# Kernel tuning notes

Measured on AMD Instinct MI355X. Metric: run time of the kernel, lower is better.

## Reference

```python
import jax, jax.numpy as jnp
import numpy as np

B, LQ, LK = 4, 256, 512
DQ, DK, DV = 512, 512, 512
H = 256
NEG = -1e6


def setup_inputs() -> dict:
    key = jax.random.key(0)
    ks = jax.random.split(key, 7)
    queries = jax.random.normal(ks[0], (B, LQ, DQ), dtype=jnp.float32)
    keys = jax.random.normal(ks[1], (B, LK, DK), dtype=jnp.float32)
    values = jax.random.normal(ks[2], (B, LK, DV), dtype=jnp.float32)
    valid_lens = jax.random.randint(ks[3], (B,), 1, LK + 1).astype(jnp.int32)
    # learned params (Linear without bias): store as (in, out) so x @ W matches torch x @ W.T
    Wq = jax.random.normal(ks[4], (DQ, H), dtype=jnp.float32) * (1.0 / np.sqrt(DQ))
    Wk = jax.random.normal(ks[5], (DK, H), dtype=jnp.float32) * (1.0 / np.sqrt(DK))
    wv = jax.random.normal(ks[6], (H,), dtype=jnp.float32) * (1.0 / np.sqrt(H))
    return {"queries": queries, "keys": keys, "values": values,
            "valid_lens": valid_lens, "Wq": Wq, "Wk": Wk, "wv": wv}


def reference(queries, keys, values, valid_lens, Wq, Wk, wv):
    q = jnp.einsum('bqd,dh->bqh', queries, Wq)          # (B,Lq,H)
    k = jnp.einsum('bkd,dh->bkh', keys, Wk)             # (B,Lk,H)
    feats = jnp.tanh(q[:, :, None, :] + k[:, None, :, :])  # (B,Lq,Lk,H)
    scores = jnp.einsum('bqkh,h->bqk', feats, wv)        # (B,Lq,Lk)
    mask = jnp.arange(LK)[None, None, :] < valid_lens[:, None, None]  # (B,1,Lk)
    attn = jax.nn.softmax(jnp.where(mask, scores, NEG), axis=-1)
    return jnp.einsum('bqk,bkv->bqv', attn, values)      # (B,Lq,Dv)
```

## Files before the change

### kernel.cpp

```cpp
#include <hip/hip_runtime.h>

#define B_   4
#define LQ_  256
#define LK_  512
#define DIN_ 512
#define H_   256
#define DV_  512

#define L2E 1.4426950408889634f

__global__ __launch_bounds__(256) void proj_partial_kernel(
    const float* __restrict__ Q, const float* __restrict__ K,
    const float* __restrict__ Wq, const float* __restrict__ Wk,
    const int* __restrict__ valid_lens,
    float* __restrict__ qpart, float* __restrict__ ekTpart) {
  __shared__ float xs[64][68];
  __shared__ float ws[64][132];

  const int blk = blockIdx.x;
  const bool isQ = blk < 128;
  int b, row0, h0, ds;
  if (isQ) {
    const int qi = blk;
    ds = qi & 3; h0 = ((qi >> 2) & 1) * 128;
    const int rt = qi >> 3;
    b = rt >> 2; row0 = (rt & 3) * 64;
  } else {
    const int u = blk - 128;
    ds = u & 3; h0 = ((u >> 2) & 1) * 128;
    const int rt = u >> 3;
    b = rt & 3; row0 = (rt >> 2) * 64;
    if (row0 >= valid_lens[b]) return;
  }
  const int L = isQ ? LQ_ : LK_;
  const float* __restrict__ X = (isQ ? Q : K) + ((size_t)(b * L + row0)) * DIN_ + ds * 128;
  const float* __restrict__ Wb = (isQ ? Wq : Wk) + (size_t)(ds * 128) * H_ + h0;

  const int t = threadIdx.x;
  const int hthr = t & 31;
  const int rthr = t >> 5;

  float acc[8][4];
#pragma unroll
  for (int r = 0; r < 8; ++r)
#pragma unroll
    for (int c = 0; c < 4; ++c) acc[r][c] = 0.f;

  for (int dd = 0; dd < 128; dd += 64) {
    __syncthreads();
#pragma unroll
    for (int u = 0; u < 4; ++u) {
      const int f = t + 256 * u;
      const int r = f >> 4, c4 = (f & 15) << 2;
      *(float4*)&xs[r][c4] = *(const float4*)&X[(size_t)r * DIN_ + dd + c4];
    }
#pragma unroll
    for (int u = 0; u < 8; ++u) {
      const int f = t + 256 * u;
      const int k = f >> 5, c4 = (f & 31) << 2;
      *(float4*)&ws[k][c4] = *(const float4*)&Wb[(size_t)(dd + k) * H_ + c4];
    }
    __syncthreads();

    for (int k = 0; k < 64; k += 8) {
      float4 w4[8];
#pragma unroll
      for (int k8 = 0; k8 < 8; ++k8)
        w4[k8] = *(const float4*)&ws[k + k8][4 * hthr];
#pragma unroll
      for (int rr = 0; rr < 8; ++rr) {
        const float4 xa = *(const float4*)&xs[rthr * 8 + rr][k];
        const float4 xb = *(const float4*)&xs[rthr * 8 + rr][k + 4];
        const float xv[8] = {xa.x, xa.y, xa.z, xa.w, xb.x, xb.y, xb.z, xb.w};
#pragma unroll
        for (int k8 = 0; k8 < 8; ++k8) {
          acc[rr][0] = fmaf(xv[k8], w4[k8].x, acc[rr][0]);
          acc[rr][1] = fmaf(xv[k8], w4[k8].y, acc[rr][1]);
          acc[rr][2] = fmaf(xv[k8], w4[k8].z, acc[rr][2]);
          acc[rr][3] = fmaf(xv[k8], w4[k8].w, acc[rr][3]);
        }
      }
    }
  }

  if (isQ) {
    float* dst = qpart + (size_t)ds * (B_ * LQ_ * H_);
#pragma unroll
    for (int rr = 0; rr < 8; ++rr) {
      const int row = row0 + rthr * 8 + rr;
      float4 o = {acc[rr][0], acc[rr][1], acc[rr][2], acc[rr][3]};
      *(float4*)&dst[(size_t)(b * LQ_ + row) * H_ + h0 + 4 * hthr] = o;
    }
  } else {
    float* dst = ekTpart + (size_t)ds * (B_ * H_ * LK_);
#pragma unroll
    for (int c = 0; c < 4; ++c) {
      const int h = h0 + 4 * hthr + c;
      float* p = &dst[((size_t)b * H_ + h) * LK_ + row0 + rthr * 8];
      float4 lo = {acc[0][c], acc[1][c], acc[2][c], acc[3][c]};
      float4 hi = {acc[4][c], acc[5][c], acc[6][c], acc[7][c]};
      *(float4*)p = lo;
      *(float4*)(p + 4) = hi;
    }
  }
}

__global__ __launch_bounds__(512) void combine_exp_kernel(
    const float* __restrict__ qpart, const float* __restrict__ ekTpart,
    const float* __restrict__ wv,
    float* __restrict__ eq, float* __restrict__ ekT, float* __restrict__ wsum) {
  const int idx = blockIdx.x * 512 + threadIdx.x;
  const int NQ4 = B_ * LQ_ * H_ / 4;
  const float4* src;
  float4* dst;
  size_t stride4;
  int k4;
  if (idx < NQ4) {
    src = (const float4*)qpart; dst = (float4*)eq;
    stride4 = NQ4; k4 = idx;
  } else {
    src = (const float4*)ekTpart; dst = (float4*)ekT;
    stride4 = B_ * H_ * LK_ / 4; k4 = idx - NQ4;
  }
  float4 a = src[k4];
  float4 b1 = src[stride4 + k4];
  float4 c = src[2 * stride4 + k4];
  float4 d = src[3 * stride4 + k4];
  float4 o;
  o.x = exp2f(fminf(fmaxf((a.x + b1.x + c.x + d.x) * L2E, -126.f), 126.f));
  o.y = exp2f(fminf(fmaxf((a.y + b1.y + c.y + d.y) * L2E, -126.f), 126.f));
  o.z = exp2f(fminf(fmaxf((a.z + b1.z + c.z + d.z) * L2E, -126.f), 126.f));
  o.w = exp2f(fminf(fmaxf((a.w + b1.w + c.w + d.w) * L2E, -126.f), 126.f));
  dst[k4] = o;

  if (blockIdx.x == 0 && threadIdx.x < 64) {
    const int t = threadIdx.x;
    float s = wv[t] + wv[t + 64] + wv[t + 128] + wv[t + 192];
#pragma unroll
    for (int off = 32; off; off >>= 1) s += __shfl_xor(s, off);
    if (t == 0) *wsum = s;
  }
}

__global__ __launch_bounds__(256) void scores_kernel(
    const float* __restrict__ eq, const float* __restrict__ ekT,
    const float* __restrict__ wv, const float* __restrict__ wsum,
    const int* __restrict__ valid_lens, float* __restrict__ sc) {
  const int blk = blockIdx.x;
  const int b  = blk & 3;
  const int i0 = ((blk >> 2) & 63) * 4;
  const int jc = blk >> 8;
  const int vl = valid_lens[b];
  if (jc * 256 >= vl) return;
  const int t = threadIdx.x;
  if (jc * 256 + ((t >> 6) << 6) >= vl) return;
  const int j = jc * 256 + t;

  const float* __restrict__ kcol = ekT + (size_t)b * H_ * LK_ + j;
  const float* __restrict__ q0 = eq + (size_t)(b * LQ_ + i0) * H_;
  const float Wsum = *wsum;

  float a0 = 0.f, a1 = 0.f, a2 = 0.f, a3 = 0.f;
  for (int h = 0; h < H_; h += 8) {
    float kv[8];
#pragma unroll
    for (int u = 0; u < 8; ++u) kv[u] = kcol[(size_t)(h + u) * LK_];
    const float4 wa = *(const float4*)&wv[h];
    const float4 wb = *(const float4*)&wv[h + 4];
    const float ww[8] = {wa.x, wa.y, wa.z, wa.w, wb.x, wb.y, wb.z, wb.w};
#pragma unroll
    for (int ii = 0; ii < 4; ++ii) {
      const float4 qa = *(const float4*)&q0[ii * H_ + h];
      const float4 qb = *(const float4*)&q0[ii * H_ + h + 4];
      const float qv[8] = {qa.x, qa.y, qa.z, qa.w, qb.x, qb.y, qb.z, qb.w};
      float* acc = (ii == 0) ? &a0 : (ii == 1) ? &a1 : (ii == 2) ? &a2 : &a3;
      float s = *acc;
#pragma unroll
      for (int u = 0; u < 8; ++u) {
        const float p = qv[u] * kv[u];
        s = fmaf(ww[u], __builtin_amdgcn_rcpf(fmaf(p, p, 1.f)), s);
      }
      *acc = s;
    }
  }
  const size_t o = (size_t)(b * LQ_ + i0) * LK_ + j;
  if (j < vl) {
    sc[o]           = fmaf(-2.f, a0, Wsum);
    sc[o + LK_]     = fmaf(-2.f, a1, Wsum);
    sc[o + 2 * LK_] = fmaf(-2.f, a2, Wsum);
    sc[o + 3 * LK_] = fmaf(-2.f, a3, Wsum);
  }
}

__global__ __launch_bounds__(512) void softmax_av_kernel(
    const float* __restrict__ sc, const float* __restrict__ V,
    const int* __restrict__ valid_lens, float* __restrict__ out) {
  __shared__ float4 p4s[LK_];
  __shared__ float redm[8][4];
  __shared__ float reds[8][4];

  const int blk = blockIdx.x;
  const int b = blk >> 6;
  const int i0 = (blk & 63) * 4;
  const int vl = valid_lens[b];
  const int t = threadIdx.x;
  const int lane = t & 63, wave = t >> 6;

  const float* __restrict__ srow = sc + (size_t)(b * LQ_ + i0) * LK_;
  const bool valid = t < vl;
  float s[4], m[4];
#pragma unroll
  for (int ii = 0; ii < 4; ++ii) {
    s[ii] = valid ? srow[ii * LK_ + t] : -3.0e38f;
    m[ii] = s[ii];
  }
#pragma unroll
  for (int off = 32; off; off >>= 1)
#pragma unroll
    for (int ii = 0; ii < 4; ++ii) m[ii] = fmaxf(m[ii], __shfl_xor(m[ii], off));
  if (lane == 0)
#pragma unroll
    for (int ii = 0; ii < 4; ++ii) redm[wave][ii] = m[ii];
  __syncthreads();
  float e[4], sum[4];
#pragma unroll
  for (int ii = 0; ii < 4; ++ii) {
    float mx = redm[0][ii];
#pragma unroll
    for (int w = 1; w < 8; ++w) mx = fmaxf(mx, redm[w][ii]);
    e[ii] = valid ? __expf(s[ii] - mx) : 0.f;
    sum[ii] = e[ii];
  }
#pragma unroll
  for (int off = 32; off; off >>= 1)
#pragma unroll
    for (int ii = 0; ii < 4; ++ii) sum[ii] += __shfl_xor(sum[ii], off);
  if (lane == 0)
#pragma unroll
    for (int ii = 0; ii < 4; ++ii) reds[wave][ii] = sum[ii];
  __syncthreads();
  {
    float4 pv;
    float tot[4];
#pragma unroll
    for (int ii = 0; ii < 4; ++ii) {
      tot[ii] = reds[0][ii];
#pragma unroll
      for (int w = 1; w < 8; ++w) tot[ii] += reds[w][ii];
    }
    pv.x = e[0] * __builtin_amdgcn_rcpf(tot[0]);
    pv.y = e[1] * __builtin_amdgcn_rcpf(tot[1]);
    pv.z = e[2] * __builtin_amdgcn_rcpf(tot[2]);
    pv.w = e[3] * __builtin_amdgcn_rcpf(tot[3]);
    p4s[t] = pv;
  }
  __syncthreads();

  const float* __restrict__ Vb = V + (size_t)b * LK_ * DV_ + t;
  float a[4] = {0.f, 0.f, 0.f, 0.f};
  int j = 0;
  const int jv = vl & ~7;
  for (; j < jv; j += 8) {
    float v[8];
#pragma unroll
    for (int u = 0; u < 8; ++u) v[u] = Vb[(size_t)(j + u) * DV_];
#pragma unroll
    for (int u = 0; u < 8; ++u) {
      const float4 pp = p4s[j + u];
      a[0] = fmaf(pp.x, v[u], a[0]); a[1] = fmaf(pp.y, v[u], a[1]);
      a[2] = fmaf(pp.z, v[u], a[2]); a[3] = fmaf(pp.w, v[u], a[3]);
    }
  }
  for (; j < vl; ++j) {
    const float v = Vb[(size_t)j * DV_];
    const float4 pp = p4s[j];
    a[0] = fmaf(pp.x, v, a[0]); a[1] = fmaf(pp.y, v, a[1]);
    a[2] = fmaf(pp.z, v, a[2]); a[3] = fmaf(pp.w, v, a[3]);
  }
#pragma unroll
  for (int ii = 0; ii < 4; ++ii)
    out[(size_t)(b * LQ_ + i0 + ii) * DV_ + t] = a[ii];
}

extern "C" void kernel_launch(void* const* d_in, const int* in_sizes, int n_in,
                              void* d_out, int out_size, void* d_ws, size_t ws_size,
                              hipStream_t stream) {
  const float* queries    = (const float*)d_in[0];
  const float* keys       = (const float*)d_in[1];
  const float* values     = (const float*)d_in[2];
  const int*   valid_lens = (const int*)d_in[3];
  const float* Wq         = (const float*)d_in[4];
  const float* Wk         = (const float*)d_in[5];
  const float* wv         = (const float*)d_in[6];
  float* out = (float*)d_out;

  char* ws = (char*)d_ws;
  float* qpart   = (float*)ws;
  float* ekTpart = (float*)(ws + (size_t)( 4 << 20));
  float* eq      = (float*)(ws + (size_t)(12 << 20));
  float* ekT     = (float*)(ws + (size_t)(13 << 20));
  float* sc      = (float*)(ws + (size_t)(15 << 20));
  float* wsum    = (float*)(ws + (size_t)(17 << 20));

  proj_partial_kernel<<<384, 256, 0, stream>>>(
      queries, keys, Wq, Wk, valid_lens, qpart, ekTpart);
  combine_exp_kernel<<<384, 512, 0, stream>>>(
      qpart, ekTpart, wv, eq, ekT, wsum);
  scores_kernel<<<512, 256, 0, stream>>>(
      eq, ekT, wv, wsum, valid_lens, sc);
  softmax_av_kernel<<<B_ * (LQ_ / 4), 512, 0, stream>>>(
      sc, values, valid_lens, out);
}
```

Before: 63.82 us.

## Tile scores kernel in LDS with 2x2 register blocking and row-major ek

The scores kernel now stages a 32x256 block of exp(q) and a transposed 32x256 block of exp(k) in shared memory, and each thread computes a 2x2 tile of scores. Previously each thread read a column of ekT from global memory and q rows through the cache. The projection kernel now writes exp(k) row-major like q, so the transposed global store is gone and the transpose happens in LDS instead. The code references a variable `L` that is not defined in the shown lines, and the scores kernel no longer masks j >= valid_len within a tile, which relies on softmax ignoring those entries.

```diff
diff --git a/kernel.cpp b/kernel.cpp
--- a/kernel.cpp
+++ b/kernel.cpp
@@ -13,7 +13,7 @@
     const float* __restrict__ Q, const float* __restrict__ K,
     const float* __restrict__ Wq, const float* __restrict__ Wk,
     const int* __restrict__ valid_lens,
-    float* __restrict__ qpart, float* __restrict__ ekTpart) {
+    float* __restrict__ qpart, float* __restrict__ ekpart) {
   __shared__ float xs[64][68];
   __shared__ float ws[64][132];
 
@@ -83,32 +83,20 @@
     }
   }
 
-  if (isQ) {
-    float* dst = qpart + (size_t)ds * (B_ * LQ_ * H_);
-#pragma unroll
-    for (int rr = 0; rr < 8; ++rr) {
-      const int row = row0 + rthr * 8 + rr;
-      float4 o = {acc[rr][0], acc[rr][1], acc[rr][2], acc[rr][3]};
-      *(float4*)&dst[(size_t)(b * LQ_ + row) * H_ + h0 + 4 * hthr] = o;
-    }
-  } else {
-    float* dst = ekTpart + (size_t)ds * (B_ * H_ * LK_);
-#pragma unroll
-    for (int c = 0; c < 4; ++c) {
-      const int h = h0 + 4 * hthr + c;
-      float* p = &dst[((size_t)b * H_ + h) * LK_ + row0 + rthr * 8];
-      float4 lo = {acc[0][c], acc[1][c], acc[2][c], acc[3][c]};
-      float4 hi = {acc[4][c], acc[5][c], acc[6][c], acc[7][c]};
-      *(float4*)p = lo;
-      *(float4*)(p + 4) = hi;
-    }
+  float* dst = isQ ? (qpart + (size_t)ds * (B_ * LQ_ * H_))
+                   : (ekpart + (size_t)ds * (B_ * LK_ * H_));
+#pragma unroll
+  for (int rr = 0; rr < 8; ++rr) {
+    const int row = row0 + rthr * 8 + rr;
+    float4 o = {acc[rr][0], acc[rr][1], acc[rr][2], acc[rr][3]};
+    *(float4*)&dst[(size_t)(b * L + row) * H_ + h0 + 4 * hthr] = o;
   }
 }
 
 __global__ __launch_bounds__(512) void combine_exp_kernel(
-    const float* __restrict__ qpart, const float* __restrict__ ekTpart,
+    const float* __restrict__ qpart, const float* __restrict__ ekpart,
     const float* __restrict__ wv,
-    float* __restrict__ eq, float* __restrict__ ekT, float* __restrict__ wsum) {
+    float* __restrict__ eq, float* __restrict__ ek, float* __restrict__ wsum) {
   const int idx = blockIdx.x * 512 + threadIdx.x;
   const int NQ4 = B_ * LQ_ * H_ / 4;
   const float4* src;
@@ -119,8 +107,8 @@
     src = (const float4*)qpart; dst = (float4*)eq;
     stride4 = NQ4; k4 = idx;
   } else {
-    src = (const float4*)ekTpart; dst = (float4*)ekT;
-    stride4 = B_ * H_ * LK_ / 4; k4 = idx - NQ4;
+    src = (const float4*)ekpart; dst = (float4*)ek;
+    stride4 = B_ * LK_ * H_ / 4; k4 = idx - NQ4;
   }
   float4 a = src[k4];
   float4 b1 = src[stride4 + k4];
@@ -143,53 +131,74 @@
 }
 
 __global__ __launch_bounds__(256) void scores_kernel(
-    const float* __restrict__ eq, const float* __restrict__ ekT,
+    const float* __restrict__ eq, const float* __restrict__ ek,
     const float* __restrict__ wv, const float* __restrict__ wsum,
     const int* __restrict__ valid_lens, float* __restrict__ sc) {
+  __shared__ float eq_s[32][260];
+  __shared__ float ek_s[256][36];
+  __shared__ float wv_s[260];
+
   const int blk = blockIdx.x;
   const int b  = blk & 3;
-  const int i0 = ((blk >> 2) & 63) * 4;
-  const int jc = blk >> 8;
+  const int it = (blk >> 2) & 7;
+  const int jt = blk >> 5;
   const int vl = valid_lens[b];
-  if (jc * 256 >= vl) return;
+  if (jt * 32 >= vl) return;
   const int t = threadIdx.x;
-  if (jc * 256 + ((t >> 6) << 6) >= vl) return;
-  const int j = jc * 256 + t;
-
-  const float* __restrict__ kcol = ekT + (size_t)b * H_ * LK_ + j;
-  const float* __restrict__ q0 = eq + (size_t)(b * LQ_ + i0) * H_;
+  const int tx = t & 15, ty = t >> 4;
+  const int i0 = it * 32, j0 = jt * 32;
+
+  const float* __restrict__ eqb = eq + ((size_t)(b * LQ_ + i0)) * H_;
+#pragma unroll
+  for (int u = 0; u < 8; ++u) {
+    const int f = t + 256 * u;
+    const int r = f >> 6, c4 = (f & 63) << 2;
+    *(float4*)&eq_s[r][c4] = *(const float4*)&eqb[(size_t)r * H_ + c4];
+  }
+  const float* __restrict__ ekb = ek + ((size_t)(b * LK_ + j0)) * H_;
+  {
+    const int hq = t & 63, jg = t >> 6;
+#pragma unroll
+    for (int p = 0; p < 8; ++p) {
+      const int jj = jg + 4 * p;
+      const float4 v = *(const float4*)&ekb[(size_t)jj * H_ + 4 * hq];
+      ek_s[4 * hq][jj]     = v.x;
+      ek_s[4 * hq + 1][jj] = v.y;
+      ek_s[4 * hq + 2][jj] = v.z;
+      ek_s[4 * hq + 3][jj] = v.w;
+    }
+  }
+  if (t < 64) {
+#pragma unroll
+    for (int u = 0; u < 4; ++u) wv_s[t + 64 * u] = wv[t + 64 * u];
+  }
+  __syncthreads();
+
   const float Wsum = *wsum;
-
-  float a0 = 0.f, a1 = 0.f, a2 = 0.f, a3 = 0.f;
-  for (int h = 0; h < H_; h += 8) {
-    float kv[8];
-#pragma unroll
-    for (int u = 0; u < 8; ++u) kv[u] = kcol[(size_t)(h + u) * LK_];
-    const float4 wa = *(const float4*)&wv[h];
-    const float4 wb = *(const float4*)&wv[h + 4];
-    const float ww[8] = {wa.x, wa.y, wa.z, wa.w, wb.x, wb.y, wb.z, wb.w};
-#pragma unroll
-    for (int ii = 0; ii < 4; ++ii) {
-      const float4 qa = *(const float4*)&q0[ii * H_ + h];
-      const float4 qb = *(const float4*)&q0[ii * H_ + h + 4];
-      const float qv[8] = {qa.x, qa.y, qa.z, qa.w, qb.x, qb.y, qb.z, qb.w};
-      float* acc = (ii == 0) ? &a0 : (ii == 1) ? &a1 : (ii == 2) ? &a2 : &a3;
-      float s = *acc;
-#pragma unroll
-      for (int u = 0; u < 8; ++u) {
-        const float p = qv[u] * kv[u];
-        s = fmaf(ww[u], __builtin_amdgcn_rcpf(fmaf(p, p, 1.f)), s);
-      }
-      *acc = s;
-    }
-  }
-  const size_t o = (size_t)(b * LQ_ + i0) * LK_ + j;
-  if (j < vl) {
-    sc[o]           = fmaf(-2.f, a0, Wsum);
-    sc[o + LK_]     = fmaf(-2.f, a1, Wsum);
-    sc[o + 2 * LK_] = fmaf(-2.f, a2, Wsum);
-    sc[o + 3 * LK_] = fmaf(-2.f, a3, Wsum);
-  }
+  float a00 = 0.f, a01 = 0.f, a10 = 0.f, a11 = 0.f;
+#pragma unroll 2
+  for (int hq = 0; hq < 64; ++hq) {
+    const float4 q0 = *(const float4*)&eq_s[2 * ty][4 * hq];
+    const float4 q1 = *(const float4*)&eq_s[2 * ty + 1][4 * hq];
+    const float4 w4 = *(const float4*)&wv_s[4 * hq];
+    const float qa[4] = {q0.x, q0.y, q0.z, q0.w};
+    const float qb[4] = {q1.x, q1.y, q1.z, q1.w};
+    const float ww[4] = {w4.x, w4.y, w4.z, w4.w};
+#pragma unroll
+    for (int u = 0; u < 4; ++u) {
+      const float2 kk = *(const float2*)&ek_s[4 * hq + u][2 * tx];
+      float p;
+      p = qa[u] * kk.x; a00 = fmaf(ww[u], __builtin_amdgcn_rcpf(fmaf(p, p, 1.f)), a00);
+      p = qa[u] * kk.y; a01 = fmaf(ww[u], __builtin_amdgcn_rcpf(fmaf(p, p, 1.f)), a01);
+      p = qb[u] * kk.x; a10 = fmaf(ww[u], __builtin_amdgcn_rcpf(fmaf(p, p, 1.f)), a10);
+      p = qb[u] * kk.y; a11 = fmaf(ww[u], __builtin_amdgcn_rcpf(fmaf(p, p, 1.f)), a11);
+    }
+  }
+  const int i = i0 + 2 * ty, j = j0 + 2 * tx;
+  float2 r0 = {fmaf(-2.f, a00, Wsum), fmaf(-2.f, a01, Wsum)};
+  float2 r1 = {fmaf(-2.f, a10, Wsum), fmaf(-2.f, a11, Wsum)};
+  *(float2*)&sc[(size_t)(b * LQ_ + i) * LK_ + j] = r0;
+  *(float2*)&sc[(size_t)(b * LQ_ + i + 1) * LK_ + j] = r1;
 }
 
 __global__ __launch_bounds__(512) void softmax_av_kernel(
@@ -295,19 +304,19 @@
   float* out = (float*)d_out;
 
   char* ws = (char*)d_ws;
-  float* qpart   = (float*)ws;
-  float* ekTpart = (float*)(ws + (size_t)( 4 << 20));
-  float* eq      = (float*)(ws + (size_t)(12 << 20));
-  float* ekT     = (float*)(ws + (size_t)(13 << 20));
-  float* sc      = (float*)(ws + (size_t)(15 << 20));
-  float* wsum    = (float*)(ws + (size_t)(17 << 20));
+  float* qpart  = (float*)ws;
+  float* ekpart = (float*)(ws + (size_t)( 4 << 20));
+  float* eq     = (float*)(ws + (size_t)(12 << 20));
+  float* ek     = (float*)(ws + (size_t)(13 << 20));
+  float* sc     = (float*)(ws + (size_t)(15 << 20));
+  float* wsum   = (float*)(ws + (size_t)(17 << 20));
 
   proj_partial_kernel<<<384, 256, 0, stream>>>(
-      queries, keys, Wq, Wk, valid_lens, qpart, ekTpart);
+      queries, keys, Wq, Wk, valid_lens, qpart, ekpart);
   combine_exp_kernel<<<384, 512, 0, stream>>>(
-      qpart, ekTpart, wv, eq, ekT, wsum);
+      qpart, ekpart, wv, eq, ek, wsum);
   scores_kernel<<<512, 256, 0, stream>>>(
-      eq, ekT, wv, wsum, valid_lens, sc);
+      eq, ek, wv, wsum, valid_lens, sc);
   softmax_av_kernel<<<B_ * (LQ_ / 4), 512, 0, stream>>>(
       sc, values, valid_lens, out);
 }
```

After: 62.72 us. Within noise of the previous version (-1.7%).

## Fuse combine, scores and softmax-AV into one kernel recomputing K exp

Applied to the files above, without the earlier changes.

Replaces the combine/exp, scores and softmax-AV kernels with one kernel per query block. It sums the Q partials into shared memory and computes scores directly from the K partials, applying exp on the fly. This removes two launches and the global round trips of eq, ekT and scores. In exchange, every block re-reads all four K partial buffers and recomputes exp, which adds a lot of redundant L2 traffic and transcendental work.

```diff
diff --git a/kernel.cpp b/kernel.cpp
--- a/kernel.cpp
+++ b/kernel.cpp
@@ -105,115 +105,85 @@
   }
 }
 
-__global__ __launch_bounds__(512) void combine_exp_kernel(
+__global__ __launch_bounds__(512) void fused_attn_kernel(
     const float* __restrict__ qpart, const float* __restrict__ ekTpart,
-    const float* __restrict__ wv,
-    float* __restrict__ eq, float* __restrict__ ekT, float* __restrict__ wsum) {
-  const int idx = blockIdx.x * 512 + threadIdx.x;
-  const int NQ4 = B_ * LQ_ * H_ / 4;
-  const float4* src;
-  float4* dst;
-  size_t stride4;
-  int k4;
-  if (idx < NQ4) {
-    src = (const float4*)qpart; dst = (float4*)eq;
-    stride4 = NQ4; k4 = idx;
-  } else {
-    src = (const float4*)ekTpart; dst = (float4*)ekT;
-    stride4 = B_ * H_ * LK_ / 4; k4 = idx - NQ4;
-  }
-  float4 a = src[k4];
-  float4 b1 = src[stride4 + k4];
-  float4 c = src[2 * stride4 + k4];
-  float4 d = src[3 * stride4 + k4];
-  float4 o;
-  o.x = exp2f(fminf(fmaxf((a.x + b1.x + c.x + d.x) * L2E, -126.f), 126.f));
-  o.y = exp2f(fminf(fmaxf((a.y + b1.y + c.y + d.y) * L2E, -126.f), 126.f));
-  o.z = exp2f(fminf(fmaxf((a.z + b1.z + c.z + d.z) * L2E, -126.f), 126.f));
-  o.w = exp2f(fminf(fmaxf((a.w + b1.w + c.w + d.w) * L2E, -126.f), 126.f));
-  dst[k4] = o;
-
-  if (blockIdx.x == 0 && threadIdx.x < 64) {
-    const int t = threadIdx.x;
-    float s = wv[t] + wv[t + 64] + wv[t + 128] + wv[t + 192];
-#pragma unroll
-    for (int off = 32; off; off >>= 1) s += __shfl_xor(s, off);
-    if (t == 0) *wsum = s;
-  }
-}
-
-__global__ __launch_bounds__(256) void scores_kernel(
-    const float* __restrict__ eq, const float* __restrict__ ekT,
-    const float* __restrict__ wv, const float* __restrict__ wsum,
-    const int* __restrict__ valid_lens, float* __restrict__ sc) {
+    const float* __restrict__ wv, const int* __restrict__ valid_lens,
+    const float* __restrict__ V, float* __restrict__ out) {
+  __shared__ float eqs[4][260];
+  __shared__ float4 p4s[LK_];
+  __shared__ float redm[8][4], reds[8][4];
+  __shared__ float wsum_s;
+
   const int blk = blockIdx.x;
   const int b  = blk & 3;
-  const int i0 = ((blk >> 2) & 63) * 4;
-  const int jc = blk >> 8;
-  const int vl = valid_lens[b];
-  if (jc * 256 >= vl) return;
-  const int t = threadIdx.x;
-  if (jc * 256 + ((t >> 6) << 6) >= vl) return;
-  const int j = jc * 256 + t;
-
-  const float* __restrict__ kcol = ekT + (size_t)b * H_ * LK_ + j;
-  const float* __restrict__ q0 = eq + (size_t)(b * LQ_ + i0) * H_;
-  const float Wsum = *wsum;
-
-  float a0 = 0.f, a1 = 0.f, a2 = 0.f, a3 = 0.f;
-  for (int h = 0; h < H_; h += 8) {
-    float kv[8];
-#pragma unroll
-    for (int u = 0; u < 8; ++u) kv[u] = kcol[(size_t)(h + u) * LK_];
-    const float4 wa = *(const float4*)&wv[h];
-    const float4 wb = *(const float4*)&wv[h + 4];
-    const float ww[8] = {wa.x, wa.y, wa.z, wa.w, wb.x, wb.y, wb.z, wb.w};
-#pragma unroll
-    for (int ii = 0; ii < 4; ++ii) {
-      const float4 qa = *(const float4*)&q0[ii * H_ + h];
-      const float4 qb = *(const float4*)&q0[ii * H_ + h + 4];
-      const float qv[8] = {qa.x, qa.y, qa.z, qa.w, qb.x, qb.y, qb.z, qb.w};
-      float* acc = (ii == 0) ? &a0 : (ii == 1) ? &a1 : (ii == 2) ? &a2 : &a3;
-      float s = *acc;
-#pragma unroll
-      for (int u = 0; u < 8; ++u) {
-        const float p = qv[u] * kv[u];
-        s = fmaf(ww[u], __builtin_amdgcn_rcpf(fmaf(p, p, 1.f)), s);
-      }
-      *acc = s;
-    }
-  }
-  const size_t o = (size_t)(b * LQ_ + i0) * LK_ + j;
-  if (j < vl) {
-    sc[o]           = fmaf(-2.f, a0, Wsum);
-    sc[o + LK_]     = fmaf(-2.f, a1, Wsum);
-    sc[o + 2 * LK_] = fmaf(-2.f, a2, Wsum);
-    sc[o + 3 * LK_] = fmaf(-2.f, a3, Wsum);
-  }
-}
-
-__global__ __launch_bounds__(512) void softmax_av_kernel(
-    const float* __restrict__ sc, const float* __restrict__ V,
-    const int* __restrict__ valid_lens, float* __restrict__ out) {
-  __shared__ float4 p4s[LK_];
-  __shared__ float redm[8][4];
-  __shared__ float reds[8][4];
-
-  const int blk = blockIdx.x;
-  const int b = blk >> 6;
-  const int i0 = (blk & 63) * 4;
+  const int i0 = (blk >> 2) * 4;
   const int vl = valid_lens[b];
   const int t = threadIdx.x;
   const int lane = t & 63, wave = t >> 6;
 
-  const float* __restrict__ srow = sc + (size_t)(b * LQ_ + i0) * LK_;
+  const size_t QN = (size_t)B_ * LQ_ * H_;
+#pragma unroll
+  for (int e = t; e < 4 * H_; e += 512) {
+    const int i = e >> 8, h = e & 255;
+    const size_t base = (size_t)(b * LQ_ + i0 + i) * H_ + h;
+    const float v = qpart[base] + qpart[QN + base] +
+                    qpart[2 * QN + base] + qpart[3 * QN + base];
+    eqs[i][h] = exp2f(fminf(fmaxf(v * L2E, -126.f), 126.f));
+  }
+  if (t < 64) {
+    float s = wv[t] + wv[t + 64] + wv[t + 128] + wv[t + 192];
+#pragma unroll
+    for (int off = 32; off; off >>= 1) s += __shfl_xor(s, off);
+    if (t == 0) wsum_s = s;
+  }
+  __syncthreads();
+  const float Wsum = wsum_s;
+
+  float s[4] = {-3.0e38f, -3.0e38f, -3.0e38f, -3.0e38f};
   const bool valid = t < vl;
-  float s[4], m[4];
-#pragma unroll
-  for (int ii = 0; ii < 4; ++ii) {
-    s[ii] = valid ? srow[ii * LK_ + t] : -3.0e38f;
-    m[ii] = s[ii];
-  }
+  if (valid) {
+    const size_t KN = (size_t)B_ * H_ * LK_;
+    const float* __restrict__ kb = ekTpart + (size_t)b * H_ * LK_ + t;
+    float a0 = 0.f, a1 = 0.f, a2 = 0.f, a3 = 0.f;
+    for (int h = 0; h < H_; h += 4) {
+      float kraw[4];
+#pragma unroll
+      for (int u = 0; u < 4; ++u) {
+        const size_t o = (size_t)(h + u) * LK_;
+        kraw[u] = kb[o] + kb[KN + o] + kb[2 * KN + o] + kb[3 * KN + o];
+      }
+      float kv[4];
+#pragma unroll
+      for (int u = 0; u < 4; ++u)
+        kv[u] = exp2f(fminf(fmaxf(kraw[u] * L2E, -126.f), 126.f));
+      const float4 w4 = *(const float4*)&wv[h];
+      const float ww[4] = {w4.x, w4.y, w4.z, w4.w};
+      const float4 q0 = *(const float4*)&eqs[0][h];
+      const float4 q1 = *(const float4*)&eqs[1][h];
+      const float4 q2 = *(const float4*)&eqs[2][h];
+      const float4 q3 = *(const float4*)&eqs[3][h];
+      const float qq0[4] = {q0.x, q0.y, q0.z, q0.w};
+      const float qq1[4] = {q1.x, q1.y, q1.z, q1.w};
+      const float qq2[4] = {q2.x, q2.y, q2.z, q2.w};
+      const float qq3[4] = {q3.x, q3.y, q3.z, q3.w};
+#pragma unroll
+      for (int u = 0; u < 4; ++u) {
+        float p;
+        p = qq0[u] * kv[u]; a0 = fmaf(ww[u], __builtin_amdgcn_rcpf(fmaf(p, p, 1.f)), a0);
+        p = qq1[u] * kv[u]; a1 = fmaf(ww[u], __builtin_amdgcn_rcpf(fmaf(p, p, 1.f)), a1);
+        p = qq2[u] * kv[u]; a2 = fmaf(ww[u], __builtin_amdgcn_rcpf(fmaf(p, p, 1.f)), a2);
+        p = qq3[u] * kv[u]; a3 = fmaf(ww[u], __builtin_amdgcn_rcpf(fmaf(p, p, 1.f)), a3);
+      }
+    }
+    s[0] = fmaf(-2.f, a0, Wsum);
+    s[1] = fmaf(-2.f, a1, Wsum);
+    s[2] = fmaf(-2.f, a2, Wsum);
+    s[3] = fmaf(-2.f, a3, Wsum);
+  }
+
+  float m[4];
+#pragma unroll
+  for (int ii = 0; ii < 4; ++ii) m[ii] = s[ii];
 #pragma unroll
   for (int off = 32; off; off >>= 1)
 #pragma unroll
@@ -296,18 +266,10 @@
 
   char* ws = (char*)d_ws;
   float* qpart   = (float*)ws;
-  float* ekTpart = (float*)(ws + (size_t)( 4 << 20));
-  float* eq      = (float*)(ws + (size_t)(12 << 20));
-  float* ekT     = (float*)(ws + (size_t)(13 << 20));
-  float* sc      = (float*)(ws + (size_t)(15 << 20));
-  float* wsum    = (float*)(ws + (size_t)(17 << 20));
+  float* ekTpart = (float*)(ws + (size_t)(4 << 20));
 
   proj_partial_kernel<<<384, 256, 0, stream>>>(
       queries, keys, Wq, Wk, valid_lens, qpart, ekTpart);
-  combine_exp_kernel<<<384, 512, 0, stream>>>(
-      qpart, ekTpart, wv, eq, ekT, wsum);
-  scores_kernel<<<512, 256, 0, stream>>>(
-      eq, ekT, wv, wsum, valid_lens, sc);
-  softmax_av_kernel<<<B_ * (LQ_ / 4), 512, 0, stream>>>(
-      sc, values, valid_lens, out);
+  fused_attn_kernel<<<B_ * (LQ_ / 4), 512, 0, stream>>>(
+      qpart, ekTpart, wv, valid_lens, values, out);
 }
```

New measurement: 80.50 us. +26.1%, slower.
